# Optimization experiments

Measured on AMD Instinct MI355X. Metric: run time of the kernel, lower is better.

Reference implementation:

```python
import jax, jax.numpy as jnp
import numpy as np

B, N, L, K, CD, H, DH, D = 2, 2048, 1024, 16, 2, 4, 128, 128
HD = H * DH  # 512
FQ = 2.0  # embedding_freq_multiplier for query-invariant embedding
FV = 2.0  # embedding_freq_multiplier for value-invariant embedding
SCALE = 1.0 / float(np.sqrt(DH))


def _ln(x, s, b, eps=1e-6):
    m = x.mean(-1, keepdims=True)
    v = x.var(-1, keepdims=True)
    return (x - m) / jnp.sqrt(v + eps) * s + b


def _ffn(x, w1, b1, ls, lb, w2, b2):
    # PointwiseFFN: Dense -> gelu -> LayerNorm -> Dense
    h = jax.nn.gelu(x @ w1 + b1)
    return _ln(h, ls, lb) @ w2 + b2


def _rff(inv, Bm, freq, w1, b1, w2, b2):
    # random-Fourier-feature embedding of the invariant, then 2-layer MLP
    proj = (2.0 * jnp.pi * freq) * (inv @ Bm)          # (..., DH//2)
    feats = jnp.concatenate([jnp.sin(proj), jnp.cos(proj)], axis=-1)  # (..., DH)
    return jax.nn.gelu(feats @ w1 + b1) @ w2 + b2      # (..., DH)


def _forward(x, p, c, window_sigma, x_h,
             rffq, rffv,
             eq_w1, eq_b1, eq_w2, eq_b2,
             ev_w1, ev_b1, ev_w2, ev_b2,
             wq, bq, wk, bk, wv, bv,
             cw1, cb1, cls, clb, cw2, cb2,
             ivw1, ivb1, ivls, ivlb, ivw2, ivb2,
             mw1, mb1, mls, mlb, mw2, mb2,
             wo, bo):
    # relative-position invariant: (B, N, L, CD)
    rel = x[:, :, None, :] - p[:, None, :, :]
    dist = jnp.linalg.norm(rel, axis=-1)                         # (B, N, L)
    nearest = jnp.argsort(dist, axis=-1)[:, :, :K]               # (B, N, K)
    inv = jnp.take_along_axis(
        rel, jnp.broadcast_to(nearest[..., None], nearest.shape + (CD,)), axis=2)  # (B,N,K,CD)
    cg = jnp.take_along_axis(c[:, None, :, :], nearest[..., None], axis=2)         # (B,N,K,D)

    q = _rff(inv, rffq, FQ, eq_w1, eq_b1, eq_w2, eq_b2) @ wq + bq  # (B,N,K,HD)
    k_ = cg @ wk + bk                                              # (B,N,K,HD)
    v = cg @ wv + bv                                               # (B,N,K,HD)

    # conditioned value transform
    inv_emb_v = _rff(inv, rffv, FV, ev_w1, ev_b1, ev_w2, ev_b2)    # (B,N,K,DH)
    gb = _ffn(x_h, cw1, cb1, cls, clb, cw2, cb2)                   # (B,N,2*DH)
    g, bt = jnp.split(gb, 2, axis=-1)
    inv_emb_v = inv_emb_v * (1 + g[:, :, None, :]) + bt[:, :, None, :]
    vgb = _ffn(inv_emb_v, ivw1, ivb1, ivls, ivlb, ivw2, ivb2)      # (B,N,K,2*HD)
    vg, vb = jnp.split(vgb, 2, axis=-1)
    v = v * (1 + vg) + vb
    v = v.reshape(v.shape[:-1] + (H, DH))                          # (B,N,K,H,DH)
    v = _ffn(v, mw1, mb1, mls, mlb, mw2, mb2)

    q = q.reshape(q.shape[:-1] + (H, DH))
    k_ = k_.reshape(k_.shape[:-1] + (H, DH))
    att = (q * k_).sum(axis=-1) * SCALE                            # (B,N,K,H)

    # gaussian window in log-space, gathered at nearest latents
    gw_full = -0.5 * (dist ** 2)[..., None] / (window_sigma[:, None, :, :] ** 2)  # (B,N,L,1)
    gw = jnp.take_along_axis(gw_full, nearest[..., None], axis=2)                  # (B,N,K,1)
    att = jax.nn.softmax(att + gw, axis=-2)                        # softmax over K

    y = (att[..., None] * v).sum(axis=2)                           # (B,N,H,DH)
    y = y.reshape(y.shape[0], y.shape[1], HD)
    return y @ wo + bo                                             # (B,N,DH)


def setup_inputs() -> dict:
    key = jax.random.key(0)
    ks = jax.random.split(key, 24)
    dn = lambda k, i, o: jax.random.normal(k, (i, o), jnp.float32) / float(np.sqrt(i))
    z = lambda n: jnp.zeros((n,), jnp.float32)
    o = lambda n: jnp.ones((n,), jnp.float32)
    inp = {
        'x': jax.random.uniform(ks[0], (B, N, CD), jnp.float32),
        'p': jax.random.uniform(ks[1], (B, L, CD), jnp.float32),
        'c': jax.random.normal(ks[2], (B, L, D), jnp.float32),
        'window_sigma': jax.random.uniform(ks[3], (B, L, 1), jnp.float32, minval=0.1, maxval=0.5),
        'x_h': jax.random.normal(ks[4], (B, N, DH), jnp.float32),
        'rffq': jax.random.normal(ks[5], (CD, DH // 2), jnp.float32),
        'rffv': jax.random.normal(ks[6], (CD, DH // 2), jnp.float32),
        'eq_w1': dn(ks[7], DH, DH), 'eq_b1': z(DH),
        'eq_w2': dn(ks[8], DH, DH), 'eq_b2': z(DH),
        'ev_w1': dn(ks[9], DH, DH), 'ev_b1': z(DH),
        'ev_w2': dn(ks[10], DH, DH), 'ev_b2': z(DH),
        'wq': dn(ks[11], DH, HD), 'bq': z(HD),
        'wk': dn(ks[12], D, HD), 'bk': z(HD),
        'wv': dn(ks[13], D, HD), 'bv': z(HD),
        'cw1': dn(ks[14], DH, DH), 'cb1': z(DH), 'cls': o(DH), 'clb': z(DH),
        'cw2': dn(ks[15], DH, 2 * DH), 'cb2': z(2 * DH),
        'ivw1': dn(ks[16], DH, DH), 'ivb1': z(DH), 'ivls': o(DH), 'ivlb': z(DH),
        'ivw2': dn(ks[17], DH, 2 * HD), 'ivb2': z(2 * HD),
        'mw1': dn(ks[18], DH, DH), 'mb1': z(DH), 'mls': o(DH), 'mlb': z(DH),
        'mw2': dn(ks[19], DH, DH), 'mb2': z(DH),
        'wo': dn(ks[20], HD, DH), 'bo': z(DH),
    }
    return inp


def reference(x, p, c, window_sigma, x_h,
              rffq, rffv,
              eq_w1, eq_b1, eq_w2, eq_b2,
              ev_w1, ev_b1, ev_w2, ev_b2,
              wq, bq, wk, bk, wv, bv,
              cw1, cb1, cls, clb, cw2, cb2,
              ivw1, ivb1, ivls, ivlb, ivw2, ivb2,
              mw1, mb1, mls, mlb, mw2, mb2,
              wo, bo):
    return _forward(x, p, c, window_sigma, x_h,
                    rffq, rffv,
                    eq_w1, eq_b1, eq_w2, eq_b2,
                    ev_w1, ev_b1, ev_w2, ev_b2,
                    wq, bq, wk, bk, wv, bv,
                    cw1, cb1, cls, clb, cw2, cb2,
                    ivw1, ivb1, ivls, ivlb, ivw2, ivb2,
                    mw1, mb1, mls, mlb, mw2, mb2,
                    wo, bo)
```

## Files before the change

kernel.cpp:

```cpp
#include <hip/hip_runtime.h>
#include <hip/hip_bf16.h>
#include <math.h>

#define Bx  2
#define Nx  2048
#define Lx  1024
#define Kx  16
#define Hx  4
#define DHx 128
#define HDx 512
#define NROW 65536

typedef unsigned short u16;
typedef unsigned int   u32;
typedef unsigned long long u64;

#define ALD 132
#define KLD 520
#define LDW 136

typedef __attribute__((ext_vector_type(8))) short bf16x8;
typedef __attribute__((ext_vector_type(4))) float f32x4;
typedef __attribute__((ext_vector_type(4))) unsigned int u32x4;

// ... 340 lines not shown
    const void* __restrict__ rffq, const void* __restrict__ rffv,
    const void* __restrict__ eqw1, const void* __restrict__ eqb1,
    const void* __restrict__ eqw2, const void* __restrict__ eqb2,
    const void* __restrict__ evw1, const void* __restrict__ evb1,
    const void* __restrict__ evw2, const void* __restrict__ evb2,
    const void* __restrict__ wq, const void* __restrict__ bq,
    const void* __restrict__ wk, const void* __restrict__ bk,
    const void* __restrict__ wv, const void* __restrict__ bv,
    const void* __restrict__ cw1, const void* __restrict__ cb1,
    const void* __restrict__ cls, const void* __restrict__ clb,
    const void* __restrict__ cw2, const void* __restrict__ cb2,
    const void* __restrict__ ivw1, const void* __restrict__ ivb1,
    const void* __restrict__ ivls, const void* __restrict__ ivlb,
    const void* __restrict__ ivw2, const void* __restrict__ ivb2,
    const void* __restrict__ mw1, const void* __restrict__ mb1,
    const void* __restrict__ mls, const void* __restrict__ mlb,
    const void* __restrict__ mw2, const void* __restrict__ mb2,
    const void* __restrict__ wo, const void* __restrict__ bo,
    const int* __restrict__ flag, void* __restrict__ outp) {
  if (*flag != ISB) return;
  __shared__ SMEM sm;
  __shared__ u64 WMIN[4];
  int t = threadIdx.x;
  int bid = blockIdx.x;
  int b = bid >> 11;
  float* bufA = sm.SA;
  float* bufB = sm.SA + 16 * ALD;

  float* DIST = sm.KV;
  float qx = ldg1<ISB>(x, bid * 2 + 0);
  float qy = ldg1<ISB>(x, bid * 2 + 1);
#pragma unroll
  for (int e = 0; e < 4; e++) {
    int l = t + e * 256;
    float px = ldg1<ISB>(p, (b * Lx + l) * 2 + 0);
    float py = ldg1<ISB>(p, (b * Lx + l) * 2 + 1);
    float dx = qx - px, dy = qy - py;
    float d2 = __fadd_rn(__fmul_rn(dx, dx), __fmul_rn(dy, dy));
    DIST[l] = __fsqrt_rn(d2);
  }
  __syncthreads();
  for (int kk = 0; kk < Kx; kk++) {
    u64 key = ~0ull;
#pragma unroll
    for (int e = 0; e < 4; e++) {
      int l = t + e * 256;
      u64 k2 = (((u64)__float_as_uint(DIST[l])) << 32) | (u32)l;
      key = key < k2 ? key : k2;
    }
#pragma unroll
    for (int off = 32; off; off >>= 1) {
      u64 o = shfl_down_u64(key, off);
      key = key < o ? key : o;
    }
    if ((t & 63) == 0) WMIN[t >> 6] = key;
    __syncthreads();
    if (t == 0) {
      u64 kmin = WMIN[0];
#pragma unroll
      for (int w = 1; w < 4; w++) kmin = kmin < WMIN[w] ? kmin : WMIN[w];
      int l = (int)(kmin & 0xffffffffu);
      float d = __uint_as_float((u32)(kmin >> 32));
      DIST[l] = __builtin_inff();
      float px = ldg1<ISB>(p, (b * Lx + l) * 2 + 0);
      float py = ldg1<ISB>(p, (b * Lx + l) * 2 + 1);
      float s  = ldg1<ISB>(sig, b * Lx + l);
      sm.IDX[kk] = l;
      sm.INVS[kk * 2 + 0] = qx - px;
      sm.INVS[kk * 2 + 1] = qy - py;
      sm.GWS[kk] = (-0.5f * (d * d)) / (s * s);
    }
    __syncthreads();
  }

  if (t < 128) sm.YV[t] = ldg1<ISB>(xh, bid * 128 + t);
  __syncthreads();
  float hacc = 0.0f;
  if (t < 128) {
    hacc = ldg1<ISB>(cb1, t);
    for (int i = 0; i < 128; i++) hacc += sm.YV[i] * ldg1<ISB>(cw1, i * 128 + t);
    hacc = geluf(hacc);
  }
  {
    float s = hacc, s2 = hacc * hacc;
#pragma unroll
    for (int off = 32; off; off >>= 1) {
      s += __shfl_down(s, off);
      s2 += __shfl_down(s2, off);
    }
    if ((t & 63) == 0) { sm.RED[(t >> 6) * 2] = s; sm.RED[(t >> 6) * 2 + 1] = s2; }
  }
  __syncthreads();
  {
    float m   = (sm.RED[0] + sm.RED[2]) * (1.0f / 128.0f);
    float var = fmaxf((sm.RED[1] + sm.RED[3]) * (1.0f / 128.0f) - m * m, 0.0f);
    float rstd = rsqrtf(var + 1e-6f);
    if (t < 128) sm.YV[128 + t] = (hacc - m) * rstd * ldg1<ISB>(cls, t) + ldg1<ISB>(clb, t);
  }
  __syncthreads();
  {
    float a = ldg1<ISB>(cb2, t);
    for (int i = 0; i < 128; i++) a += sm.YV[128 + i] * ldg1<ISB>(cw2, i * 256 + t);
    if (t < 128) sm.GV[t] = a; else sm.BT[t - 128] = a;
  }
  __syncthreads();

  {
    int r = t >> 4, c8 = (t & 15) * 8;
    int li = sm.IDX[r];
    ldg8<ISB>(c, (b * Lx + li) * 128 + c8, sm.CG + r * ALD + c8);
  }
  __syncthreads();

#pragma unroll
  for (int pp = 0; pp < 4; pp++) {
    int idx = t + pp * 256;
    int r = idx >> 6, cc = idx & 63;
    float proj = 12.566370614359172f *
                 (sm.INVS[r * 2] * ldg1<ISB>(rffq, cc) +
                  sm.INVS[r * 2 + 1] * ldg1<ISB>(rffq, 64 + cc));
    bufA[r * ALD + cc]      = sinf(proj);
    bufA[r * ALD + 64 + cc] = cosf(proj);
  }
  __syncthreads();
  gemm128<ISB>(bufA, eqw1, 128, eqb1, bufB, 1, t); __syncthreads();
  gemm128<ISB>(bufB, eqw2, 128, eqb2, bufA, 0, t); __syncthreads();

  gemm512<ISB>(sm.CG, wk, bk, sm.KV, t); __syncthreads();

  for (int h = 0; h < 4; h++) {
    gemm128<ISB>(bufA, (const void*)((const char*)wq + (ISB ? 2 : 4) * (size_t)(h * 128)), 512,
                 (const void*)((const char*)bq + (ISB ? 2 : 4) * (size_t)(h * 128)), bufB, 0, t);
    __syncthreads();
    int r = t >> 4, seg = t & 15;
    float s = 0.0f;
    const float* qp = bufB + r * ALD + seg * 8;
    const float* kp = sm.KV + r * KLD + h * 128 + seg * 8;
#pragma unroll
    for (int e = 0; e < 8; e++) s += qp[e] * kp[e];
    sm.RED[r * 16 + seg] = s;
    __syncthreads();
    if (t < 16) {
      float ss = 0.0f;
      for (int e = 0; e < 16; e++) ss += sm.RED[t * 16 + e];
      sm.ATT[t * 4 + h] = ss * 0.08838834764831845f;
    }
    __syncthreads();
  }

  gemm512<ISB>(sm.CG, wv, bv, sm.KV, t); __syncthreads();

#pragma unroll
  for (int pp = 0; pp < 4; pp++) {
    int idx = t + pp * 256;
    int r = idx >> 6, cc = idx & 63;
    float proj = 12.566370614359172f *
                 (sm.INVS[r * 2] * ldg1<ISB>(rffv, cc) +
                  sm.INVS[r * 2 + 1] * ldg1<ISB>(rffv, 64 + cc));
    bufA[r * ALD + cc]      = sinf(proj);
    bufA[r * ALD + 64 + cc] = cosf(proj);
  }
  __syncthreads();
  gemm128<ISB>(bufA, evw1, 128, evb1, bufB, 1, t); __syncthreads();
  gemm128<ISB>(bufB, evw2, 128, evb2, bufA, 0, t); __syncthreads();

#pragma unroll
  for (int pp = 0; pp < 8; pp++) {
    int idx = t + pp * 256;
    int r = idx >> 7, cc = idx & 127;
    bufA[r * ALD + cc] = bufA[r * ALD + cc] * (1.0f + sm.GV[cc]) + sm.BT[cc];
  }
  __syncthreads();
  gemm128<ISB>(bufA, ivw1, 128, ivb1, bufB, 1, t); __syncthreads();
  ln_vecs<16, ISB>(bufB, ALD, ivls, ivlb, sm.YV, sm.RED, t); __syncthreads();

  ivw2_fuse<ISB>(bufB, ivw2, ivb2, sm.KV, 0, t);
  ivw2_fuse<ISB>(bufB, ivw2, ivb2, sm.KV, 8, t);
  __syncthreads();

  for (int pass = 0; pass < 2; pass++) {
    mm_from_kv<ISB>(sm.KV, mw1, mb1, sm.SA, pass * 32, t); __syncthreads();
    ln_vecs<32, ISB>(sm.SA, ALD, mls, mlb, sm.YV, sm.RED, t); __syncthreads();
    mm_to_kv<ISB>(sm.SA, mw2, mb2, sm.KV, pass * 32, t); __syncthreads();
  }

  if (t < 4) {
    float mx = -1e30f;
    for (int r = 0; r < 16; r++) {
      float v = sm.ATT[r * 4 + t] + sm.GWS[r];
      mx = fmaxf(mx, v);
    }
    float ssum = 0.0f;
    float ev[16];
    for (int r = 0; r < 16; r++) {
      float e = expf(sm.ATT[r * 4 + t] + sm.GWS[r] - mx);
      ev[r] = e; ssum += e;
    }
    float inv = 1.0f / fmaxf(ssum, 1e-37f);
    for (int r = 0; r < 16; r++) sm.ATT[r * 4 + t] = ev[r] * inv;
  }
  __syncthreads();

#pragma unroll
  for (int pp = 0; pp < 2; pp++) {
    int j = t + pp * 256;
    int h = j >> 7;
    float s = 0.0f;
    for (int r = 0; r < 16; r++) s += sm.ATT[r * 4 + h] * sm.KV[r * KLD + j];
    sm.YV[j] = s;
  }
  __syncthreads();

  if (t < 128) {
    float s = ldg1<ISB>(bo, t);
    for (int j = 0; j < 512; j++) s += sm.YV[j] * ldg1<ISB>(wo, j * 128 + t);
    stg1<ISB>(outp, bid * 128 + t, s);
  }
}


#define OFF_WQ    0
#define OFF_WK    65536
#define OFF_WV    131072
#define OFF_IVW2  196608
#define OFF_EQW1  327680
#define OFF_EQW2  344064
#define OFF_EVW1  360448
#define OFF_EVW2  376832
#define OFF_IVW1  393216
#define OFF_MW1   409600
#define OFF_MW2   425984
#define OFF_CW1   442368
#define OFF_CW2   458752
#define OFF_WO    491520
#define WT_TOTAL  557056

__device__ __attribute__((aligned(16))) u16 g_wth[WT_TOTAL];
__device__ __attribute__((aligned(16))) u16 g_wtl[WT_TOTAL];

__device__ __attribute__((aligned(16))) u16 gAh[NROW * 128], gAl[NROW * 128];
__device__ __attribute__((aligned(16))) u16 gBh[4096 * 128], gBl[4096 * 128];
__device__ __attribute__((aligned(16))) u16 gCGh[NROW * 128], gCGl[NROW * 128];
__device__ __attribute__((aligned(16))) u16 gVHh[NROW * 128], gVHl[NROW * 128];
__device__ __attribute__((aligned(16))) u16 gEIh[NROW * 128], gEIl[NROW * 128];
__device__ float gY[4096 * 512];
__device__ float gGVBT[4096 * 256];
__device__ float gATT[4096 * 64];
__device__ float gINVS[4096 * 32];
__device__ float gGWS[4096 * 16];
__device__ int   gIDX[NROW];

__global__ void k_prep32(
    const void* wq, const void* wk, const void* wv, const void* ivw2,
    const void* eqw1, const void* eqw2, const void* evw1, const void* evw2,
    const void* ivw1, const void* mw1, const void* mw2,
    const void* cw1, const void* cw2, const void* wo,
    const int* __restrict__ flag) {
  if (*flag != 0) return;
  int gid = blockIdx.x * 256 + threadIdx.x;
  float w;
  if (gid >= OFF_WO) {
    int local = gid - OFF_WO;
    int n = local >> 9, k = local & 511;
    w = ((const float*)wo)[k * 128 + n];
  } else {
    const float* src; int N; int local;
    if      (gid < OFF_WK)   { src = (const float*)wq;   N = 512;  local = gid - OFF_WQ; }
    else if (gid < OFF_WV)   { src = (const float*)wk;   N = 512;  local = gid - OFF_WK; }
    else if (gid < OFF_IVW2) { src = (const float*)wv;   N = 512;  local = gid - OFF_WV; }
    else if (gid < OFF_EQW1) { src = (const float*)ivw2; N = 1024; local = gid - OFF_IVW2; }
    else if (gid < OFF_EQW2) { src = (const float*)eqw1; N = 128;  local = gid - OFF_EQW1; }
    else if (gid < OFF_EVW1) { src = (const float*)eqw2; N = 128;  local = gid - OFF_EQW2; }
    else if (gid < OFF_EVW2) { src = (const float*)evw1; N = 128;  local = gid - OFF_EVW1; }
    else if (gid < OFF_IVW1) { src = (const float*)evw2; N = 128;  local = gid - OFF_EVW2; }
    else if (gid < OFF_MW1)  { src = (const float*)ivw1; N = 128;  local = gid - OFF_IVW1; }
    else if (gid < OFF_MW2)  { src = (const float*)mw1;  N = 128;  local = gid - OFF_MW1; }
    else if (gid < OFF_CW1)  { src = (const float*)mw2;  N = 128;  local = gid - OFF_MW2; }
    else if (gid < OFF_CW2)  { src = (const float*)cw1;  N = 128;  local = gid - OFF_CW1; }
    else                     { src = (const float*)cw2;  N = 256;  local = gid - OFF_CW2; }
    int n = local >> 7, k = local & 127;
    w = src[k * N + n];
  }
  u16 h = f2bf(w);
  g_wth[gid] = h;
  g_wtl[gid] = f2bf(w - bf(h));
}

__device__ __forceinline__ f32x4 mfma16(bf16x8 a, bf16x8 b, f32x4 c) {
  return __builtin_amdgcn_mfma_f32_16x16x32_bf16(a, b, c, 0, 0, 0);
}

__device__ __forceinline__ void stageW(
    const u16* __restrict__ wth, const u16* __restrict__ wtl, int srcStride,
    u16* __restrict__ sWh, u16* __restrict__ sWl, int t) {
#pragma unroll
  for (int it = 0; it < 4; it++) {
    int i = t + it * 512;
    int row = i >> 4, c8 = (i & 15) * 8;
    *(uint4*)(sWh + row * LDW + c8) = *(const uint4*)(wth + (size_t)row * srcStride + c8);
    *(uint4*)(sWl + row * LDW + c8) = *(const uint4*)(wtl + (size_t)row * srcStride + c8);
  }
}

__device__ __forceinline__ void loadA(
    const u16* __restrict__ Ah, const u16* __restrict__ Al, size_t abase,
    int lane, bf16x8 ah[4], bf16x8 al[4]) {
  int r = lane & 15, kg = lane >> 4;
#pragma unroll
  for (int kc = 0; kc < 4; kc++) {
    ah[kc] = *(const bf16x8*)(Ah + abase + (size_t)r * 128 + kc * 32 + kg * 8);
    al[kc] = *(const bf16x8*)(Al + abase + (size_t)r * 128 + kc * 32 + kg * 8);
  }
}

__device__ __forceinline__ void loadA_nt(
    const u16* __restrict__ Ah, const u16* __restrict__ Al, size_t abase,
    int lane, bf16x8 ah[4], bf16x8 al[4]) {
  int r = lane & 15, kg = lane >> 4;
#pragma unroll
  for (int kc = 0; kc < 4; kc++) {
    ah[kc] = ntload8(Ah + abase + (size_t)r * 128 + kc * 32 + kg * 8);
    al[kc] = ntload8(Al + abase + (size_t)r * 128 + kc * 32 + kg * 8);
  }
}

__device__ __forceinline__ void loadA_lds(
    const u16* __restrict__ sAh_w, const u16* __restrict__ sAl_w,
    int lane, bf16x8 ah[4], bf16x8 al[4]) {
  int r = lane & 15, kg = lane >> 4;
#pragma unroll
  for (int kc = 0; kc < 4; kc++) {
    ah[kc] = *(const bf16x8*)(sAh_w + r * LDW + kc * 32 + kg * 8);
    al[kc] = *(const bf16x8*)(sAl_w + r * LDW + kc * 32 + kg * 8);
  }
}

__device__ __forceinline__ void core16L(
    const bf16x8 ah[4], const bf16x8 al[4],
    const u16* __restrict__ sWh, const u16* __restrict__ sWl,
    f32x4 acc[8], int lane) {
  int r = lane & 15, kg = lane >> 4;
#pragma unroll
  for (int tile = 0; tile < 8; tile++) {
    int cc = tile * 16 + r;
    f32x4 a = {0.f, 0.f, 0.f, 0.f};
#pragma unroll
    for (int kc = 0; kc < 4; kc++) {
      bf16x8 bh = *(const bf16x8*)(sWh + cc * LDW + kc * 32 + kg * 8);
      bf16x8 bl = *(const bf16x8*)(sWl + cc * LDW + kc * 32 + kg * 8);
      a = mfma16(ah[kc], bh, a);
      a = mfma16(ah[kc], bl, a);
      a = mfma16(al[kc], bh, a);
    }
    acc[tile] = a;
  }
}

__device__ __forceinline__ void storeACT(
    f32x4 acc[8], const float* __restrict__ bias, int act,
    u16* __restrict__ sAh_w, u16* __restrict__ sAl_w, int lane) {
  int r = lane & 15, kg = lane >> 4;
#pragma unroll
  for (int tile = 0; tile < 8; tile++) {
    int cc = tile * 16 + r;
    float bc = bias[cc];
#pragma unroll
    for (int q = 0; q < 4; q++) {
      float v = acc[tile][q] + bc;
      if (act) v = geluf(v);
      int o = (kg * 4 + q) * LDW + cc;
      split2(v, sAh_w + o, sAl_w + o);
    }
  }
}

__device__ __forceinline__ void storeACT_ln(
    f32x4 acc[8], const float* __restrict__ bias,
    const float* __restrict__ sc, const float* __restrict__ bi,
    u16* __restrict__ sAh_w, u16* __restrict__ sAl_w, int lane) {
  int r = lane & 15, kg = lane >> 4;
  float v[8][4];
  float s[4] = {0.f, 0.f, 0.f, 0.f}, s2[4] = {0.f, 0.f, 0.f, 0.f};
#pragma unroll
  for (int tile = 0; tile < 8; tile++) {
    float bc = bias[tile * 16 + r];
#pragma unroll
    for (int q = 0; q < 4; q++) {
      float x = geluf(acc[tile][q] + bc);
      v[tile][q] = x; s[q] += x; s2[q] += x * x;
    }
  }
#pragma unroll
  for (int m = 1; m <= 8; m <<= 1) {
#pragma unroll
    for (int q = 0; q < 4; q++) {
      s[q]  += __shfl_xor(s[q], m);
      s2[q] += __shfl_xor(s2[q], m);
    }
  }
  float mean[4], rstd[4];
#pragma unroll
  for (int q = 0; q < 4; q++) {
    float m_ = s[q] * (1.f / 128.f);
    float var = fmaxf(s2[q] * (1.f / 128.f) - m_ * m_, 0.f);
    mean[q] = m_; rstd[q] = rsqrtf(var + 1e-6f);
  }
#pragma unroll
  for (int tile = 0; tile < 8; tile++) {
    int cc = tile * 16 + r;
    float scv = sc[cc], biv = bi[cc];
#pragma unroll
    for (int q = 0; q < 4; q++) {
      int o = (kg * 4 + q) * LDW + cc;
      split2((v[tile][q] - mean[q]) * rstd[q] * scv + biv, sAh_w + o, sAl_w + o);
    }
  }
}

__device__ __forceinline__ void store16_gelu_ln(
    f32x4 acc[8], const float* __restrict__ bias,
    const float* __restrict__ sc, const float* __restrict__ bi,
    u16* __restrict__ Oh, u16* __restrict__ Ol, size_t obase, int lane) {
  int r = lane & 15, kg = lane >> 4;
  float v[8][4];
  float s[4] = {0.f, 0.f, 0.f, 0.f}, s2[4] = {0.f, 0.f, 0.f, 0.f};
#pragma unroll
  for (int tile = 0; tile < 8; tile++) {
    float bc = bias[tile * 16 + r];
#pragma unroll
    for (int q = 0; q < 4; q++) {
      float x = geluf(acc[tile][q] + bc);
      v[tile][q] = x; s[q] += x; s2[q] += x * x;
    }
  }
#pragma unroll
  for (int m = 1; m <= 8; m <<= 1) {
#pragma unroll
    for (int q = 0; q < 4; q++) {
      s[q]  += __shfl_xor(s[q], m);
      s2[q] += __shfl_xor(s2[q], m);
    }
  }
  float mean[4], rstd[4];
#pragma unroll
  for (int q = 0; q < 4; q++) {
    float m_ = s[q] * (1.f / 128.f);
    float var = fmaxf(s2[q] * (1.f / 128.f) - m_ * m_, 0.f);
    mean[q] = m_; rstd[q] = rsqrtf(var + 1e-6f);
  }
#pragma unroll
  for (int tile = 0; tile < 8; tile++) {
    int cc = tile * 16 + r;
    float scv = sc[cc], biv = bi[cc];
#pragma unroll
    for (int q = 0; q < 4; q++) {
      size_t o = obase + (size_t)(kg * 4 + q) * 128 + cc;
      split2((v[tile][q] - mean[q]) * rstd[q] * scv + biv, Oh + o, Ol + o);
    }
  }
}


__global__ __launch_bounds__(256) void k_topk(
    const float* __restrict__ x, const float* __restrict__ p,
    const float* __restrict__ sig, const int* __restrict__ flag) {
  if (*flag != 0) return;
  int t = threadIdx.x, lane = t & 63, w = t >> 6;
  int n = blockIdx.x * 4 + w, b = n >> 11;
  float qx = x[n * 2 + 0], qy = x[n * 2 + 1];
  u64 keys[16];
#pragma unroll
  for (int e = 0; e < 16; e++) {
    int l = e * 64 + lane;
    float px = p[(b * Lx + l) * 2 + 0];
    float py = p[(b * Lx + l) * 2 + 1];
    float dx = qx - px, dy = qy - py;
    float d2 = __fadd_rn(__fmul_rn(dx, dx), __fmul_rn(dy, dy));
    keys[e] = (((u64)__float_as_uint(__fsqrt_rn(d2))) << 32) | (u32)l;
  }
#pragma unroll 1
  for (int kk = 0; kk < Kx; kk++) {
    u64 kmin = keys[0];
#pragma unroll
    for (int e = 1; e < 16; e++) kmin = kmin < keys[e] ? kmin : keys[e];
#pragma unroll
    for (int m = 1; m <= 32; m <<= 1) {
      u64 o = shfl_xor_u64(kmin, m);
      kmin = kmin < o ? kmin : o;
    }
    if (lane == 0) {
      int l = (int)(kmin & 0xffffffffu);
      float d = __uint_as_float((u32)(kmin >> 32));
      float px = p[(b * Lx + l) * 2 + 0];
      float py = p[(b * Lx + l) * 2 + 1];
      float sg = sig[b * Lx + l];
      gIDX[n * 16 + kk] = l;
      gINVS[n * 32 + kk * 2 + 0] = qx - px;
      gINVS[n * 32 + kk * 2 + 1] = qy - py;
      gGWS[n * 16 + kk] = (-0.5f * (d * d)) / (sg * sg);
    }
#pragma unroll
    for (int e = 0; e < 16; e++) if (keys[e] == kmin) keys[e] = ~0ull;
  }
}

__global__ __launch_bounds__(512, 1) void k_c1(
    const float* __restrict__ xh, const float* __restrict__ cb1,
    const float* __restrict__ cls, const float* __restrict__ clb,
    const int* __restrict__ flag) {
  if (*flag != 0) return;
  __shared__ u16 sWh[128 * LDW], sWl[128 * LDW];
  int t = threadIdx.x, lane = t & 63, w = t >> 6;
  stageW(g_wth + OFF_CW1, g_wtl + OFF_CW1, 128, sWh, sWl, t);
  size_t rb = (size_t)blockIdx.x * 128 + w * 16;
  int r = lane & 15, kg = lane >> 4;
  bf16x8 ah[4], al[4];
#pragma unroll
  for (int kc = 0; kc < 4; kc++) {
    const float* src = xh + (rb + r) * 128 + kc * 32 + kg * 8;
#pragma unroll
    for (int e = 0; e < 8; e++) {
      float xv = src[e];
      u16 hh = f2bf(xv);
      ah[kc][e] = (short)hh;
      al[kc][e] = (short)f2bf(xv - bf(hh));
    }
  }
  __syncthreads();
  f32x4 acc[8];
  core16L(ah, al, sWh, sWl, acc, lane);
  store16_gelu_ln(acc, cb1, cls, clb, gBh, gBl, rb * 128, lane);
}

__global__ __launch_bounds__(512, 1) void k_c2(
    const float* __restrict__ cb2, const int* __restrict__ flag) {
  if (*flag != 0) return;
  __shared__ u16 sWh[128 * LDW], sWl[128 * LDW];
  int t = threadIdx.x, lane = t & 63, w = t >> 6;
  size_t rb = (size_t)blockIdx.x * 128 + w * 16;
  int r = lane & 15, kg = lane >> 4;
  bf16x8 ah[4], al[4];
  loadA(gBh, gBl, rb * 128, lane, ah, al);
#pragma unroll 1
  for (int half = 0; half < 2; half++) {
    stageW(g_wth + OFF_CW2 + half * 128 * 128,
           g_wtl + OFF_CW2 + half * 128 * 128, 128, sWh, sWl, t);
    __syncthreads();
    f32x4 acc[8];
    core16L(ah, al, sWh, sWl, acc, lane);
#pragma unroll
    for (int tile = 0; tile < 8; tile++) {
      int cc = half * 128 + tile * 16 + r;
      float bc = cb2[cc];
#pragma unroll
      for (int q = 0; q < 4; q++)
        gGVBT[(rb + kg * 4 + q) * 256 + cc] = acc[tile][q] + bc;
    }
    __syncthreads();
  }
}

__global__ __launch_bounds__(512) void k_gather(
    const float* __restrict__ c, const float* __restrict__ rffq,
    const float* __restrict__ rffv, const int* __restrict__ flag) {
  if (*flag != 0) return;
  int t = threadIdx.x;
  size_t row = (size_t)blockIdx.x * 64 + (t >> 3);
  int cbase = (t & 7) * 16;
  int n = (int)(row >> 4), b = n >> 11;
  int li = gIDX[row];
  const float* cp = c + ((size_t)(b * Lx + li)) * 128 + cbase;
  float ix = gINVS[n * 32 + (row & 15) * 2 + 0];
  float iy = gINVS[n * 32 + (row & 15) * 2 + 1];
  size_t o = row * 128 + cbase;
#pragma unroll
  for (int half = 0; half < 2; half++) {
    float4 va = ((const float4*)cp)[half * 2 + 0];
    float4 vb = ((const float4*)cp)[half * 2 + 1];
    float cv[8] = {va.x, va.y, va.z, va.w, vb.x, vb.y, vb.z, vb.w};
    bf16x8 ch_, cl_, qh_, ql_, eh_, el_;
#pragma unroll
    for (int j = 0; j < 8; j++) {
      int col = cbase + half * 8 + j, cc = col & 63;
      u16 hh = f2bf(cv[j]);
      ch_[j] = (short)hh; cl_[j] = (short)f2bf(cv[j] - bf(hh));
      float pq = 12.566370614359172f * (ix * rffq[cc] + iy * rffq[64 + cc]);
      float pv = 12.566370614359172f * (ix * rffv[cc] + iy * rffv[64 + cc]);
      float vq = (col < 64) ? sinf(pq) : cosf(pq);
      float vv = (col < 64) ? sinf(pv) : cosf(pv);
      u16 qh16 = f2bf(vq);
      qh_[j] = (short)qh16; ql_[j] = (short)f2bf(vq - bf(qh16));
      u16 eh16 = f2bf(vv);
      eh_[j] = (short)eh16; el_[j] = (short)f2bf(vv - bf(eh16));
    }
    *(bf16x8*)(gCGh + o + half * 8) = ch_;
    *(bf16x8*)(gCGl + o + half * 8) = cl_;
    *(bf16x8*)(gAh  + o + half * 8) = qh_;
    *(bf16x8*)(gAl  + o + half * 8) = ql_;
    *(bf16x8*)(gVHh + o + half * 8) = eh_;
    *(bf16x8*)(gVHl + o + half * 8) = el_;
  }
}

__global__ __launch_bounds__(512, 1) void k_qatt(
    const float* __restrict__ eqb1, const float* __restrict__ eqb2,
    const float* __restrict__ bq, const float* __restrict__ bk,
    const int* __restrict__ flag) {
  if (*flag != 0) return;
  __shared__ u16 sWh[128 * LDW], sWl[128 * LDW];
  __shared__ u16 sAh[128 * LDW], sAl[128 * LDW];
  int t = threadIdx.x, lane = t & 63, w = t >> 6;
  size_t rb = (size_t)blockIdx.x * 128 + w * 16;
  u16* myAh = sAh + (w * 16) * LDW;
  u16* myAl = sAl + (w * 16) * LDW;
  int r = lane & 15, kg = lane >> 4;
  stageW(g_wth + OFF_EQW1, g_wtl + OFF_EQW1, 128, sWh, sWl, t);
  bf16x8 ah[4], al[4];
  loadA_nt(gAh, gAl, rb * 128, lane, ah, al);
  __syncthreads();
  f32x4 acc[8];
  core16L(ah, al, sWh, sWl, acc, lane);
  storeACT(acc, eqb1, 1, myAh, myAl, lane);
  __syncthreads();
  stageW(g_wth + OFF_EQW2, g_wtl + OFF_EQW2, 128, sWh, sWl, t);
  __syncthreads();
  loadA_lds(myAh, myAl, lane, ah, al);
  core16L(ah, al, sWh, sWl, acc, lane);
  storeACT(acc, eqb2, 0, myAh, myAl, lane);
  bf16x8 qfh[4], qfl[4], ckh[4], ckl[4];
  loadA_lds(myAh, myAl, lane, qfh, qfl);
  loadA_nt(gCGh, gCGl, rb * 128, lane, ckh, ckl);
  int pt = blockIdx.x * 8 + w;
#pragma unroll 1
  for (int h = 0; h < 4; h++) {
    __syncthreads();
    stageW(g_wth + OFF_WQ + h * 16384, g_wtl + OFF_WQ + h * 16384, 128, sWh, sWl, t);
    __syncthreads();
    f32x4 dq[8];
    core16L(qfh, qfl, sWh, sWl, dq, lane);
    __syncthreads();
    stageW(g_wth + OFF_WK + h * 16384, g_wtl + OFF_WK + h * 16384, 128, sWh, sWl, t);
    __syncthreads();
    float pr[4] = {0.f, 0.f, 0.f, 0.f};
#pragma unroll
    for (int tile = 0; tile < 8; tile++) {
      int cc = tile * 16 + r;
      f32x4 dk = {0.f, 0.f, 0.f, 0.f};
#pragma unroll
      for (int kc = 0; kc < 4; kc++) {
        bf16x8 bh = *(const bf16x8*)(sWh + cc * LDW + kc * 32 + kg * 8);
        bf16x8 bl = *(const bf16x8*)(sWl + cc * LDW + kc * 32 + kg * 8);
        dk = mfma16(ckh[kc], bh, dk);
        dk = mfma16(ckh[kc], bl, dk);
        dk = mfma16(ckl[kc], bh, dk);
      }
      float bqv = bq[h * 128 + cc], bkv = bk[h * 128 + cc];
#pragma unroll
      for (int q = 0; q < 4; q++)
        pr[q] += (dq[tile][q] + bqv) * (dk[q] + bkv);
    }
#pragma unroll
    for (int m = 1; m <= 8; m <<= 1) {
#pragma unroll
      for (int q = 0; q < 4; q++) pr[q] += __shfl_xor(pr[q], m);
    }
    if (r == 0) {
#pragma unroll
      for (int q = 0; q < 4; q++)
        gATT[pt * 64 + h * 16 + kg * 4 + q] = pr[q] * 0.08838834764831845f;
    }
  }
}

__global__ __launch_bounds__(256) void k_soft(const int* __restrict__ flag) {
  if (*flag != 0) return;
  int id = blockIdx.x * 256 + threadIdx.x;
  int pt = id >> 2, h = id & 3;
  float mx = -1e30f;
  for (int k = 0; k < 16; k++) {
    float v = gATT[pt * 64 + h * 16 + k] + gGWS[pt * 16 + k];
    mx = fmaxf(mx, v);
  }
  float ssum = 0.0f;
  float ev[16];
  for (int k = 0; k < 16; k++) {
    float e = expf(gATT[pt * 64 + h * 16 + k] + gGWS[pt * 16 + k] - mx);
    ev[k] = e; ssum += e;
  }
  float inv = 1.0f / fmaxf(ssum, 1e-37f);
  for (int k = 0; k < 16; k++) gATT[pt * 64 + h * 16 + k] = ev[k] * inv;
}

__global__ __launch_bounds__(512, 1) void k_echain(
    const float* __restrict__ evb1, const float* __restrict__ evb2,
    const float* __restrict__ ivb1, const float* __restrict__ ivls,
    const float* __restrict__ ivlb, const int* __restrict__ flag) {
  if (*flag != 0) return;
  __shared__ u16 sWh[128 * LDW], sWl[128 * LDW];
  __shared__ u16 sAh[128 * LDW], sAl[128 * LDW];
  int t = threadIdx.x, lane = t & 63, w = t >> 6;
  size_t rb = (size_t)blockIdx.x * 128 + w * 16;
  u16* myAh = sAh + (w * 16) * LDW;
  u16* myAl = sAl + (w * 16) * LDW;
  int r = lane & 15, kg = lane >> 4;
  int pt = blockIdx.x * 8 + w;
  stageW(g_wth + OFF_EVW1, g_wtl + OFF_EVW1, 128, sWh, sWl, t);
  bf16x8 ah[4], al[4];
  loadA_nt(gVHh, gVHl, rb * 128, lane, ah, al);
  __syncthreads();
  f32x4 acc[8];
  core16L(ah, al, sWh, sWl, acc, lane);
  storeACT(acc, evb1, 1, myAh, myAl, lane);
  __syncthreads();
  stageW(g_wth + OFF_EVW2, g_wtl + OFF_EVW2, 128, sWh, sWl, t);
  __syncthreads();
  loadA_lds(myAh, myAl, lane, ah, al);
  core16L(ah, al, sWh, sWl, acc, lane);
#pragma unroll
  for (int tile = 0; tile < 8; tile++) {
    int cc = tile * 16 + r;
    float bc = evb2[cc];
    float gv = gGVBT[pt * 256 + cc];
    float bt = gGVBT[pt * 256 + 128 + cc];
#pragma unroll
    for (int q = 0; q < 4; q++) {
      float v = (acc[tile][q] + bc) * (1.0f + gv) + bt;
      int o = (kg * 4 + q) * LDW + cc;
      split2(v, myAh + o, myAl + o);
    }
  }
  __syncthreads();
  stageW(g_wth + OFF_IVW1, g_wtl + OFF_IVW1, 128, sWh, sWl, t);
  __syncthreads();
  loadA_lds(myAh, myAl, lane, ah, al);
  core16L(ah, al, sWh, sWl, acc, lane);
  store16_gelu_ln(acc, ivb1, ivls, ivlb, gEIh, gEIl, rb * 128, lane);
}

__global__ __launch_bounds__(512, 1) void k_vchain(
    const float* __restrict__ bv, const float* __restrict__ ivb2,
    const float* __restrict__ mb1, const float* __restrict__ mls,
    const float* __restrict__ mlb, const float* __restrict__ mb2,
    const int* __restrict__ flag) {
  if (*flag != 0) return;
  __shared__ u16 sWh[128 * LDW], sWl[128 * LDW];
  __shared__ u16 sAh[128 * LDW], sAl[128 * LDW];
  int t = threadIdx.x, lane = t & 63, w = t >> 6;
  size_t rb = (size_t)blockIdx.x * 128 + w * 16;
  u16* myAh = sAh + (w * 16) * LDW;
  u16* myAl = sAl + (w * 16) * LDW;
  int r = lane & 15, kg = lane >> 4;
  int pt = blockIdx.x * 8 + w;
  bf16x8 ckh[4], ckl[4], eih[4], eil[4];
  loadA_nt(gCGh, gCGl, rb * 128, lane, ckh, ckl);
  loadA_nt(gEIh, gEIl, rb * 128, lane, eih, eil);
#pragma unroll 1
  for (int h = 0; h < 4; h++) {
    __syncthreads();
    stageW(g_wth + OFF_WV + (size_t)(h * 128) * 128,
           g_wtl + OFF_WV + (size_t)(h * 128) * 128, 128, sWh, sWl, t);
    __syncthreads();
    f32x4 vv[8];
    core16L(ckh, ckl, sWh, sWl, vv, lane);
    __syncthreads();
    stageW(g_wth + OFF_IVW2 + (size_t)(h * 128) * 128,
           g_wtl + OFF_IVW2 + (size_t)(h * 128) * 128, 128, sWh, sWl, t);
    __syncthreads();
    f32x4 ag[8];
    core16L(eih, eil, sWh, sWl, ag, lane);
    __syncthreads();
    stageW(g_wth + OFF_IVW2 + (size_t)(512 + h * 128) * 128,
           g_wtl + OFF_IVW2 + (size_t)(512 + h * 128) * 128, 128, sWh, sWl, t);
    __syncthreads();
#pragma unroll
    for (int tile = 0; tile < 8; tile++) {
      int cc = tile * 16 + r;
      f32x4 ab = {0.f, 0.f, 0.f, 0.f};
#pragma unroll
      for (int kc = 0; kc < 4; kc++) {
        bf16x8 bh = *(const bf16x8*)(sWh + cc * LDW + kc * 32 + kg * 8);
        bf16x8 bl = *(const bf16x8*)(sWl + cc * LDW + kc * 32 + kg * 8);
        ab = mfma16(eih[kc], bh, ab);
        ab = mfma16(eih[kc], bl, ab);
        ab = mfma16(eil[kc], bh, ab);
      }
      float bvv = bv[h * 128 + cc];
      float bgv = ivb2[h * 128 + cc], bbv = ivb2[512 + h * 128 + cc];
#pragma unroll
      for (int q = 0; q < 4; q++) {
        float x = vv[tile][q] + bvv;
        u16 hh = f2bf(x);
        u16 ll = f2bf(x - bf(hh));
        float v = bf(hh) + bf(ll);
        float nv = v * (1.f + (ag[tile][q] + bgv)) + (ab[q] + bbv);
        int o = (kg * 4 + q) * LDW + cc;
        split2(nv, myAh + o, myAl + o);
      }
    }
    __syncthreads();
    stageW(g_wth + OFF_MW1, g_wtl + OFF_MW1, 128, sWh, sWl, t);
    __syncthreads();
    bf16x8 vh_[4], vl_[4];
    loadA_lds(myAh, myAl, lane, vh_, vl_);
    f32x4 acc[8];
    core16L(vh_, vl_, sWh, sWl, acc, lane);
    storeACT_ln(acc, mb1, mls, mlb, myAh, myAl, lane);
    __syncthreads();
    stageW(g_wth + OFF_MW2, g_wtl + OFF_MW2, 128, sWh, sWl, t);
    __syncthreads();
    loadA_lds(myAh, myAl, lane, vh_, vl_);
    core16L(vh_, vl_, sWh, sWl, acc, lane);
    float attv[4];
#pragma unroll
    for (int q = 0; q < 4; q++) attv[q] = gATT[pt * 64 + h * 16 + kg * 4 + q];
#pragma unroll
    for (int tile = 0; tile < 8; tile++) {
      int cc = tile * 16 + r;
      float mb = mb2[cc];
      float s = 0.f;
#pragma unroll
      for (int q = 0; q < 4; q++) s += attv[q] * (acc[tile][q] + mb);
      s += __shfl_xor(s, 16);
      s += __shfl_xor(s, 32);
      if (kg == 0) gY[(size_t)pt * 512 + h * 128 + cc] = s;
    }
  }
}

__global__ __launch_bounds__(512, 1) void k_out(
    const float* __restrict__ bo, const int* __restrict__ flag,
    float* __restrict__ outp) {
  if (*flag != 0) return;
  __shared__ u16 sWh[128 * LDW], sWl[128 * LDW];
  int t = threadIdx.x, lane = t & 63, w = t >> 6;
  size_t rb = (size_t)blockIdx.x * 128 + w * 16;
  int r = lane & 15, kg = lane >> 4;
  f32x4 acc[8] = {};
#pragma unroll 1
  for (int kb = 0; kb < 4; kb++) {
    stageW(g_wth + OFF_WO + kb * 128, g_wtl + OFF_WO + kb * 128, 512, sWh, sWl, t);
    bf16x8 ah[4], al[4];
#pragma unroll
    for (int kc = 0; kc < 4; kc++) {
      const float* src = gY + (rb + r) * 512 + kb * 128 + kc * 32 + kg * 8;
#pragma unroll
      for (int e = 0; e < 8; e++) {
        float xv = src[e];
        u16 hh = f2bf(xv);
        ah[kc][e] = (short)hh;
        al[kc][e] = (short)f2bf(xv - bf(hh));
      }
    }
    __syncthreads();
#pragma unroll
    for (int tile = 0; tile < 8; tile++) {
      int cc = tile * 16 + r;
      f32x4 a = acc[tile];
#pragma unroll
      for (int kc = 0; kc < 4; kc++) {
        bf16x8 bh = *(const bf16x8*)(sWh + cc * LDW + kc * 32 + kg * 8);
        bf16x8 bl = *(const bf16x8*)(sWl + cc * LDW + kc * 32 + kg * 8);
        a = mfma16(ah[kc], bh, a);
        a = mfma16(ah[kc], bl, a);
        a = mfma16(al[kc], bh, a);
      }
      acc[tile] = a;
    }
    __syncthreads();
  }
#pragma unroll
  for (int tile = 0; tile < 8; tile++) {
    int cc = tile * 16 + r;
    float bc = bo[cc];
#pragma unroll
    for (int q = 0; q < 4; q++)
      outp[(rb + kg * 4 + q) * 128 + cc] = acc[tile][q] + bc;
  }
}

extern "C" void kernel_launch(void* const* d_in, const int* in_sizes, int n_in,
                              void* d_out, int out_size, void* d_ws, size_t ws_size,
                              hipStream_t stream) {
  (void)in_sizes; (void)n_in; (void)out_size; (void)ws_size;
  int* flag = (int*)d_ws;

  k_sniff<<<1, 64, 0, stream>>>(d_in[23], flag);

  k_prep32<<<WT_TOTAL / 256, 256, 0, stream>>>(
      d_in[15], d_in[17], d_in[19], d_in[31],
      d_in[7], d_in[9], d_in[11], d_in[13],
      d_in[27], d_in[33], d_in[37],
      d_in[21], d_in[25], d_in[39], flag);

  k_topk<<<1024, 256, 0, stream>>>((const float*)d_in[0], (const float*)d_in[1],
                                   (const float*)d_in[3], flag);
  k_c1<<<32, 512, 0, stream>>>((const float*)d_in[4], (const float*)d_in[22],
                               (const float*)d_in[23], (const float*)d_in[24], flag);
  k_c2<<<32, 512, 0, stream>>>((const float*)d_in[26], flag);
  k_gather<<<1024, 512, 0, stream>>>((const float*)d_in[2], (const float*)d_in[5],
                                     (const float*)d_in[6], flag);
  k_qatt<<<512, 512, 0, stream>>>((const float*)d_in[8], (const float*)d_in[10],
                                  (const float*)d_in[16], (const float*)d_in[18], flag);
  k_soft<<<64, 256, 0, stream>>>(flag);
  k_echain<<<512, 512, 0, stream>>>((const float*)d_in[12], (const float*)d_in[14],
                                    (const float*)d_in[28], (const float*)d_in[29],
                                    (const float*)d_in[30], flag);
  k_vchain<<<512, 512, 0, stream>>>((const float*)d_in[20], (const float*)d_in[32],
                                    (const float*)d_in[34], (const float*)d_in[35],
                                    (const float*)d_in[36], (const float*)d_in[38], flag);
  k_out<<<32, 512, 0, stream>>>((const float*)d_in[40], flag, (float*)d_out);

  k_fused<1><<<Bx * Nx, 256, 0, stream>>>(
      d_in[0], d_in[1], d_in[2], d_in[3], d_in[4], d_in[5], d_in[6],
      d_in[7], d_in[8], d_in[9], d_in[10],
      d_in[11], d_in[12], d_in[13], d_in[14],
      d_in[15], d_in[16], d_in[17], d_in[18], d_in[19], d_in[20],
      d_in[21], d_in[22], d_in[23], d_in[24], d_in[25], d_in[26],
      d_in[27], d_in[28], d_in[29], d_in[30], d_in[31], d_in[32],
      d_in[33], d_in[34], d_in[35], d_in[36], d_in[37], d_in[38],
      d_in[39], d_in[40], flag, d_out);
}
```

Before: 766.5 us.

## Prefetch next weight tile into registers while computing current stage

Replaces the synchronous global-to-LDS weight staging with a register double-buffer. The next stage's weight tile is loaded into registers right after the current tile is written to LDS, so global load latency overlaps the MFMA work. This costs about 32 extra VGPRs per thread in kernels that already hold many fragments at 512 threads, which could cause spills.

```diff
diff --git a/kernel.cpp b/kernel.cpp
--- a/kernel.cpp
+++ b/kernel.cpp
@@ -666,6 +666,28 @@
   }
 }
 
+struct WReg { uint4 h[4], l[4]; };
+__device__ __forceinline__ void wload(
+    WReg& wr, const u16* __restrict__ wth, const u16* __restrict__ wtl, int t) {
+#pragma unroll
+  for (int it = 0; it < 4; it++) {
+    int i = t + it * 512;
+    int row = i >> 4, c8 = (i & 15) * 8;
+    wr.h[it] = *(const uint4*)(wth + (size_t)row * 128 + c8);
+    wr.l[it] = *(const uint4*)(wtl + (size_t)row * 128 + c8);
+  }
+}
+__device__ __forceinline__ void wstore(
+    const WReg& wr, u16* __restrict__ sWh, u16* __restrict__ sWl, int t) {
+#pragma unroll
+  for (int it = 0; it < 4; it++) {
+    int i = t + it * 512;
+    int row = i >> 4, c8 = (i & 15) * 8;
+    *(uint4*)(sWh + row * LDW + c8) = wr.h[it];
+    *(uint4*)(sWl + row * LDW + c8) = wr.l[it];
+  }
+}
+
 __device__ __forceinline__ void loadA(
     const u16* __restrict__ Ah, const u16* __restrict__ Al, size_t abase,
     int lane, bf16x8 ah[4], bf16x8 al[4]) {
@@ -978,15 +1000,19 @@
   u16* myAh = sAh + (w * 16) * LDW;
   u16* myAl = sAl + (w * 16) * LDW;
   int r = lane & 15, kg = lane >> 4;
-  stageW(g_wth + OFF_EQW1, g_wtl + OFF_EQW1, 128, sWh, sWl, t);
+  WReg wr;
+  wload(wr, g_wth + OFF_EQW1, g_wtl + OFF_EQW1, t);
+  wstore(wr, sWh, sWl, t);
   bf16x8 ah[4], al[4];
   loadA_nt(gAh, gAl, rb * 128, lane, ah, al);
+  wload(wr, g_wth + OFF_EQW2, g_wtl + OFF_EQW2, t);
   __syncthreads();
   f32x4 acc[8];
   core16L(ah, al, sWh, sWl, acc, lane);
   storeACT(acc, eqb1, 1, myAh, myAl, lane);
   __syncthreads();
-  stageW(g_wth + OFF_EQW2, g_wtl + OFF_EQW2, 128, sWh, sWl, t);
+  wstore(wr, sWh, sWl, t);
+  wload(wr, g_wth + OFF_WQ, g_wtl + OFF_WQ, t);
   __syncthreads();
   loadA_lds(myAh, myAl, lane, ah, al);
   core16L(ah, al, sWh, sWl, acc, lane);
@@ -998,12 +1024,15 @@
 #pragma unroll 1
   for (int h = 0; h < 4; h++) {
     __syncthreads();
-    stageW(g_wth + OFF_WQ + h * 16384, g_wtl + OFF_WQ + h * 16384, 128, sWh, sWl, t);
+    wstore(wr, sWh, sWl, t);
+    wload(wr, g_wth + OFF_WK + h * 16384, g_wtl + OFF_WK + h * 16384, t);
     __syncthreads();
     f32x4 dq[8];
     core16L(qfh, qfl, sWh, sWl, dq, lane);
     __syncthreads();
-    stageW(g_wth + OFF_WK + h * 16384, g_wtl + OFF_WK + h * 16384, 128, sWh, sWl, t);
+    wstore(wr, sWh, sWl, t);
+    if (h < 3) wload(wr, g_wth + OFF_WQ + (h + 1) * 16384,
+                     g_wtl + OFF_WQ + (h + 1) * 16384, t);
     __syncthreads();
     float pr[4] = {0.f, 0.f, 0.f, 0.f};
 #pragma unroll
@@ -1068,15 +1097,19 @@
   u16* myAl = sAl + (w * 16) * LDW;
   int r = lane & 15, kg = lane >> 4;
   int pt = blockIdx.x * 8 + w;
-  stageW(g_wth + OFF_EVW1, g_wtl + OFF_EVW1, 128, sWh, sWl, t);
+  WReg wr;
+  wload(wr, g_wth + OFF_EVW1, g_wtl + OFF_EVW1, t);
+  wstore(wr, sWh, sWl, t);
   bf16x8 ah[4], al[4];
   loadA_nt(gVHh, gVHl, rb * 128, lane, ah, al);
+  wload(wr, g_wth + OFF_EVW2, g_wtl + OFF_EVW2, t);
   __syncthreads();
   f32x4 acc[8];
   core16L(ah, al, sWh, sWl, acc, lane);
   storeACT(acc, evb1, 1, myAh, myAl, lane);
   __syncthreads();
-  stageW(g_wth + OFF_EVW2, g_wtl + OFF_EVW2, 128, sWh, sWl, t);
+  wstore(wr, sWh, sWl, t);
+  wload(wr, g_wth + OFF_IVW1, g_wtl + OFF_IVW1, t);
   __syncthreads();
   loadA_lds(myAh, myAl, lane, ah, al);
   core16L(ah, al, sWh, sWl, acc, lane);
@@ -1094,7 +1127,7 @@
     }
   }
   __syncthreads();
-  stageW(g_wth + OFF_IVW1, g_wtl + OFF_IVW1, 128, sWh, sWl, t);
+  wstore(wr, sWh, sWl, t);
   __syncthreads();
   loadA_lds(myAh, myAl, lane, ah, al);
   core16L(ah, al, sWh, sWl, acc, lane);
@@ -1118,23 +1151,27 @@
   bf16x8 ckh[4], ckl[4], eih[4], eil[4];
   loadA_nt(gCGh, gCGl, rb * 128, lane, ckh, ckl);
   loadA_nt(gEIh, gEIl, rb * 128, lane, eih, eil);
+  WReg wr;
+  wload(wr, g_wth + OFF_WV, g_wtl + OFF_WV, t);
 #pragma unroll 1
   for (int h = 0; h < 4; h++) {
     __syncthreads();
-    stageW(g_wth + OFF_WV + (size_t)(h * 128) * 128,
-           g_wtl + OFF_WV + (size_t)(h * 128) * 128, 128, sWh, sWl, t);
+    wstore(wr, sWh, sWl, t);
+    wload(wr, g_wth + OFF_IVW2 + (size_t)(h * 128) * 128,
+          g_wtl + OFF_IVW2 + (size_t)(h * 128) * 128, t);
     __syncthreads();
     f32x4 vv[8];
     core16L(ckh, ckl, sWh, sWl, vv, lane);
     __syncthreads();
-    stageW(g_wth + OFF_IVW2 + (size_t)(h * 128) * 128,
-           g_wtl + OFF_IVW2 + (size_t)(h * 128) * 128, 128, sWh, sWl, t);
+    wstore(wr, sWh, sWl, t);
+    wload(wr, g_wth + OFF_IVW2 + (size_t)(512 + h * 128) * 128,
+          g_wtl + OFF_IVW2 + (size_t)(512 + h * 128) * 128, t);
     __syncthreads();
     f32x4 ag[8];
     core16L(eih, eil, sWh, sWl, ag, lane);
     __syncthreads();
-    stageW(g_wth + OFF_IVW2 + (size_t)(512 + h * 128) * 128,
-           g_wtl + OFF_IVW2 + (size_t)(512 + h * 128) * 128, 128, sWh, sWl, t);
+    wstore(wr, sWh, sWl, t);
+    wload(wr, g_wth + OFF_MW1, g_wtl + OFF_MW1, t);
     __syncthreads();
 #pragma unroll
     for (int tile = 0; tile < 8; tile++) {
@@ -1162,7 +1199,8 @@
       }
     }
     __syncthreads();
-    stageW(g_wth + OFF_MW1, g_wtl + OFF_MW1, 128, sWh, sWl, t);
+    wstore(wr, sWh, sWl, t);
+    wload(wr, g_wth + OFF_MW2, g_wtl + OFF_MW2, t);
     __syncthreads();
     bf16x8 vh_[4], vl_[4];
     loadA_lds(myAh, myAl, lane, vh_, vl_);
@@ -1170,7 +1208,9 @@
     core16L(vh_, vl_, sWh, sWl, acc, lane);
     storeACT_ln(acc, mb1, mls, mlb, myAh, myAl, lane);
     __syncthreads();
-    stageW(g_wth + OFF_MW2, g_wtl + OFF_MW2, 128, sWh, sWl, t);
+    wstore(wr, sWh, sWl, t);
+    if (h < 3) wload(wr, g_wth + OFF_WV + (size_t)((h + 1) * 128) * 128,
+                     g_wtl + OFF_WV + (size_t)((h + 1) * 128) * 128, t);
     __syncthreads();
     loadA_lds(myAh, myAl, lane, vh_, vl_);
     core16L(vh_, vl_, sWh, sWl, acc, lane);
```

Result: slower. 973.7 us (+27.0%).
